# Optimization experiments

Hardware: AMD Instinct MI355X
Metric: run time of the kernel (lower is better)

The kernel has to match this reference:

```python
import jax, jax.numpy as jnp
import numpy as np

N = 50000
E = 800000
IN_C, HID, OUT_C = 128, 64, 64
L = 8
ALPHA, THETA = 0.1, 0.5


def setup_inputs() -> dict:
    key = jax.random.key(0)
    ks = jax.random.split(key, 7)
    x = jax.random.normal(ks[0], (N, IN_C), dtype=jnp.float32)
    edge_index = jax.random.randint(ks[1], (2, E), 0, N, dtype=jnp.int64)
    # parameters (Linear weights stored [out, in] like torch)
    w_in = jax.random.normal(ks[2], (HID, IN_C), dtype=jnp.float32) / np.sqrt(IN_C)
    b_in = jnp.zeros((HID,), dtype=jnp.float32)
    conv_w = jax.random.normal(ks[3], (L, HID, HID), dtype=jnp.float32) / np.sqrt(HID)
    w_out = jax.random.normal(ks[4], (OUT_C, HID), dtype=jnp.float32) / np.sqrt(HID)
    b_out = jnp.zeros((OUT_C,), dtype=jnp.float32)
    return {"x": x, "edge_index": edge_index, "w_in": w_in, "b_in": b_in,
            "conv_w": conv_w, "w_out": w_out, "b_out": b_out}


def reference(x, edge_index, w_in, b_in, conv_w, w_out, b_out):
    # add self loops
    loops = jnp.arange(N, dtype=edge_index.dtype)
    row = jnp.concatenate([edge_index[0], loops])
    col = jnp.concatenate([edge_index[1], loops])
    # symmetric GCN normalization from in-degree of col
    deg = jax.ops.segment_sum(jnp.ones_like(col, dtype=x.dtype), col, num_segments=N)
    dinv = jnp.where(deg > 0, jax.lax.rsqrt(deg), 0.0)
    norm = (dinv[row] * dinv[col])[:, None]  # [E+N, 1]

    # eval mode: dropout is identity
    h = jax.nn.relu(x @ w_in.T + b_in)
    x0 = h
    betas = jnp.log(THETA / jnp.arange(1, L + 1, dtype=jnp.float32) + 1.0)

    def layer(h, wb):
        W, beta = wb
        agg = jax.ops.segment_sum(h[row] * norm, col, num_segments=N)  # gather-scale-scatter
        agg = (1.0 - ALPHA) * agg + ALPHA * x0                         # initial residual
        out = (1.0 - beta) * agg + beta * (agg @ W.T)                  # identity mapping
        return jax.nn.relu(out), None

    h, _ = jax.lax.scan(layer, h, (conv_w, betas))
    return h @ w_out.T + b_out
```

## Files before the change

kernel.cpp:

```cpp
#include <hip/hip_runtime.h>
#include <math.h>

#define NN 50000
#define EE 800000
#define INC 128
#define HIDC 64
#define OUTC 64
#define LLAYERS 8
#define TOT (EE + NN)
#define NB 196
#define ABLK 256
#define CHUNKA ((TOT + ABLK - 1) / ABLK)

#define WAVE_LDS_FENCE() asm volatile("s_waitcnt lgkmcnt(0)" ::: "memory")

typedef __attribute__((ext_vector_type(8))) short bf16x8;
typedef __attribute__((ext_vector_type(4))) float f32x4;

__device__ __forceinline__ float bf2f(unsigned short u) {
    return __uint_as_float(((unsigned int)u) << 16);
}
__device__ __forceinline__ unsigned short f2bf(float f) {
    unsigned int u = __float_as_uint(f);
    u += 0x7FFFu + ((u >> 16) & 1u);
    return (unsigned short)(u >> 16);
}

__global__ void detect_kernel(const long long* __restrict__ p, int* __restrict__ flag) {
    long long v = p[threadIdx.x];
    if (v < 0 || v >= NN) atomicOr(flag, 1);
}

__device__ __forceinline__ int load_row(const void* ei, int is64, int e) {
    return is64 ? (int)((const long long*)ei)[e] : ((const int*)ei)[e];
}
__device__ __forceinline__ int load_col(const void* ei, int is64, int e) {
    return is64 ? (int)((const long long*)ei)[EE + e] : ((const int*)ei)[EE + e];
}

__global__ __launch_bounds__(256) void histA(const void* __restrict__ ei,
                                             const int* __restrict__ flag,
                                             int* __restrict__ bcnt) {
    __shared__ int h[NB];
    int tid = threadIdx.x;
    for (int i = tid; i < NB; i += 256) h[i] = 0;
    __syncthreads();
    int is64 = (*flag == 0);
    int lo = blockIdx.x * CHUNKA, hi = lo + CHUNKA; if (hi > TOT) hi = TOT;
    for (int e = lo + tid; e < hi; e += 256) {
        int c = (e < EE) ? load_col(ei, is64, e) : (e - EE);
        atomicAdd(&h[c >> 8], 1);
    }
    __syncthreads();
    for (int i = tid; i < NB; i += 256) if (h[i]) atomicAdd(&bcnt[i], h[i]);
}

__global__ __launch_bounds__(256) void scan_buckets(const int* __restrict__ bcnt,
                                                    int* __restrict__ bstart,
                                                    int* __restrict__ bcur) {
    __shared__ int s[256];
    int t = threadIdx.x;
    int v = (t < NB) ? bcnt[t] : 0;
    s[t] = v;
    __syncthreads();
    for (int off = 1; off < 256; off <<= 1) {
        int a = (t >= off) ? s[t - off] : 0;
        __syncthreads();
        s[t] += a;
        __syncthreads();
    }
    if (t < NB) { int st = s[t] - v; bstart[t] = st; bcur[t] = st; }
    if (t == NB - 1) bstart[NB] = s[t];
}

__global__ __launch_bounds__(256) void bucket_scatter(const void* __restrict__ ei,
                                                      const int* __restrict__ flag,
                                                      int* __restrict__ bcur,
                                                      unsigned int* __restrict__ barr) {
    __shared__ int h[NB];
    __shared__ int base[NB];
    int tid = threadIdx.x;
    for (int i = tid; i < NB; i += 256) h[i] = 0;
    __syncthreads();
    int is64 = (*flag == 0);
    int lo = blockIdx.x * CHUNKA, hi = lo + CHUNKA; if (hi > TOT) hi = TOT;
    for (int e = lo + tid; e < hi; e += 256) {
        int c = (e < EE) ? load_col(ei, is64, e) : (e - EE);
        atomicAdd(&h[c >> 8], 1);
    }
    __syncthreads();
    for (int i = tid; i < NB; i += 256) {
        int cnt = h[i];
        base[i] = cnt ? atomicAdd(&bcur[i], cnt) : 0;
        h[i] = 0;
    }
    __syncthreads();
    for (int e = lo + tid; e < hi; e += 256) {
        int r, c;
        if (e < EE) { r = load_row(ei, is64, e); c = load_col(ei, is64, e); }
        else        { r = e - EE; c = r; }
        int b = c >> 8;
        int p = base[b] + atomicAdd(&h[b], 1);
        barr[p] = ((unsigned int)r << 8) | (unsigned int)(c & 255);
    }
}

__global__ __launch_bounds__(256) void bucket_offsets(const unsigned int* __restrict__ barr,
                                                      const int* __restrict__ bstart,
                                                      int* __restrict__ offsets,
                                                      float* __restrict__ dinv) {
    __shared__ int cnt[256];
    __shared__ int pre[256];
    int b = blockIdx.x, t = threadIdx.x;
    cnt[t] = 0;
    __syncthreads();
    int lo = bstart[b], hi = bstart[b + 1];
    for (int i = lo + t; i < hi; i += 256) atomicAdd(&cnt[barr[i] & 255u], 1);
    __syncthreads();
    int v = cnt[t];
    pre[t] = v;
    __syncthreads();
    for (int off = 1; off < 256; off <<= 1) {
        int a = (t >= off) ? pre[t - off] : 0;
        __syncthreads();
        pre[t] += a;
        __syncthreads();
    }
    int c = (b << 8) + t;
    if (c <= NN) offsets[c] = bstart[b] + pre[t] - v;
    if (c < NN)  dinv[c] = 1.0f / sqrtf((float)v);
}

__global__ __launch_bounds__(256) void bucket_place(const unsigned int* __restrict__ barr,
                                                    const int* __restrict__ bstart,
                                                    const int* __restrict__ offsets,
                                                    const float* __restrict__ dinv,
                                                    int2* __restrict__ adj) {
    __shared__ int cur[256];
    int b = blockIdx.x, t = threadIdx.x;
    int c0 = b << 8;
    int c = c0 + t;
    cur[t] = (c < NN) ? offsets[c] : 0;
    __syncthreads();
    int lo = bstart[b], hi = bstart[b + 1];
    for (int i = lo + t; i < hi; i += 256) {
        unsigned int v = barr[i];
        int r = (int)(v >> 8);
        int ci = (int)(v & 255u);
        int pos = atomicAdd(&cur[ci], 1);
        adj[pos] = make_int2(r, __float_as_int(dinv[r] * dinv[c0 + ci]));
    }
}

__global__ __launch_bounds__(256) void in_gemm(const float* __restrict__ x,
                                               const float* __restrict__ w_in,
                                               const float* __restrict__ b_in,
                                               unsigned short* __restrict__ h,
                                               float* __restrict__ x0) {
    __shared__ unsigned short xT[16 * 136];
    int tid = threadIdx.x, w = tid >> 6, lane = tid & 63;
    int g = lane >> 4, c = lane & 15;
    int base = blockIdx.x << 4;

    bf16x8 bfrag[4];
    {
        const float* Wrow = w_in + (size_t)((w << 4) + c) * INC;
        #pragma unroll
        for (int kt = 0; kt < 4; ++kt) {
            int k0 = kt * 32 + (g << 3);
            float4 va = *reinterpret_cast<const float4*>(Wrow + k0);
            float4 vb = *reinterpret_cast<const float4*>(Wrow + k0 + 4);
            bf16x8 r;
            r[0] = (short)f2bf(va.x); r[1] = (short)f2bf(va.y);
            r[2] = (short)f2bf(va.z); r[3] = (short)f2bf(va.w);
            r[4] = (short)f2bf(vb.x); r[5] = (short)f2bf(vb.y);
            r[6] = (short)f2bf(vb.z); r[7] = (short)f2bf(vb.w);
            bfrag[kt] = r;
        }
    }

    #pragma unroll
    for (int m = 0; m < 2; ++m) {
        int idx = tid * 2 + m;
        int row = idx >> 5, col4 = idx & 31;
        float4 v = *reinterpret_cast<const float4*>(
            x + (((size_t)(base + row)) << 7) + (col4 << 2));
        ushort4 pk;
        pk.x = f2bf(v.x); pk.y = f2bf(v.y); pk.z = f2bf(v.z); pk.w = f2bf(v.w);
        *reinterpret_cast<ushort4*>(&xT[row * 136 + (col4 << 2)]) = pk;
    }
    __syncthreads();

    f32x4 d = {0.f, 0.f, 0.f, 0.f};
    #pragma unroll
    for (int kt = 0; kt < 4; ++kt) {
        bf16x8 a = *reinterpret_cast<const bf16x8*>(&xT[c * 136 + kt * 32 + (g << 3)]);
        d = __builtin_amdgcn_mfma_f32_16x16x32_bf16(a, bfrag[kt], d, 0, 0, 0);
    }
    float bj = b_in[(w << 4) + c];
    #pragma unroll
    for (int r = 0; r < 4; ++r) {
        int node = base + (g << 2) + r;
        int ch = (w << 4) + c;
        float v = fmaxf(d[r] + bj, 0.0f);
        h[((size_t)node << 6) + ch]  = f2bf(v);
        x0[((size_t)node << 6) + ch] = v;
    }
}

__global__ __launch_bounds__(256) void layer_mfma(
        const unsigned short* __restrict__ h_in, unsigned short* __restrict__ h_out,
        const float* __restrict__ x0,
        const int* __restrict__ offsets, const int2* __restrict__ adj,
        const float* __restrict__ W, float beta) {
    __shared__ unsigned short WtL[64 * 72];
    __shared__ unsigned short aggT[4][16 * 72];
    int tid = threadIdx.x, w = tid >> 6, lane = tid & 63;
    int g = lane >> 4, c = lane & 15;
    float omb = 1.0f - beta;

    for (int i = tid; i < HIDC * HIDC; i += 256) {
        int n = i >> 6, k = i & 63;
        float t = beta * W[i] + ((k == n) ? omb : 0.0f);
        WtL[n * 72 + k] = f2bf(t);
    }
    __syncthreads();

    int base = blockIdx.x << 4;
    int n = base + (w << 2) + g;
    int e0 = offsets[n], e1 = offsets[n + 1];
    float4 acc = make_float4(0.f, 0.f, 0.f, 0.f);
    int e = e0;
    for (; e + 4 <= e1; e += 4) {
        int2 a0 = adj[e], a1 = adj[e + 1], a2 = adj[e + 2], a3 = adj[e + 3];
        ushort4 h0 = *reinterpret_cast<const ushort4*>(h_in + ((a0.x << 6) + (c << 2)));
        ushort4 h1 = *reinterpret_cast<const ushort4*>(h_in + ((a1.x << 6) + (c << 2)));
        ushort4 h2 = *reinterpret_cast<const ushort4*>(h_in + ((a2.x << 6) + (c << 2)));
        ushort4 h3 = *reinterpret_cast<const ushort4*>(h_in + ((a3.x << 6) + (c << 2)));
        float n0 = __int_as_float(a0.y), n1 = __int_as_float(a1.y);
        float n2 = __int_as_float(a2.y), n3 = __int_as_float(a3.y);
        acc.x = fmaf(n0, bf2f(h0.x), acc.x); acc.y = fmaf(n0, bf2f(h0.y), acc.y);
        acc.z = fmaf(n0, bf2f(h0.z), acc.z); acc.w = fmaf(n0, bf2f(h0.w), acc.w);
        acc.x = fmaf(n1, bf2f(h1.x), acc.x); acc.y = fmaf(n1, bf2f(h1.y), acc.y);
        acc.z = fmaf(n1, bf2f(h1.z), acc.z); acc.w = fmaf(n1, bf2f(h1.w), acc.w);
        acc.x = fmaf(n2, bf2f(h2.x), acc.x); acc.y = fmaf(n2, bf2f(h2.y), acc.y);
        acc.z = fmaf(n2, bf2f(h2.z), acc.z); acc.w = fmaf(n2, bf2f(h2.w), acc.w);
        acc.x = fmaf(n3, bf2f(h3.x), acc.x); acc.y = fmaf(n3, bf2f(h3.y), acc.y);
        acc.z = fmaf(n3, bf2f(h3.z), acc.z); acc.w = fmaf(n3, bf2f(h3.w), acc.w);
    }
    for (; e < e1; ++e) {
        int2 a = adj[e];
        ushort4 hv = *reinterpret_cast<const ushort4*>(h_in + ((a.x << 6) + (c << 2)));
        float nrm = __int_as_float(a.y);
        acc.x = fmaf(nrm, bf2f(hv.x), acc.x);
        acc.y = fmaf(nrm, bf2f(hv.y), acc.y);
        acc.z = fmaf(nrm, bf2f(hv.z), acc.z);
        acc.w = fmaf(nrm, bf2f(hv.w), acc.w);
    }
    {
        const float4 x0v = *reinterpret_cast<const float4*>(x0 + ((n << 6) + (c << 2)));
        ushort4 pk;
        pk.x = f2bf(fmaf(0.9f, acc.x, 0.1f * x0v.x));
        pk.y = f2bf(fmaf(0.9f, acc.y, 0.1f * x0v.y));
        pk.z = f2bf(fmaf(0.9f, acc.z, 0.1f * x0v.z));
        pk.w = f2bf(fmaf(0.9f, acc.w, 0.1f * x0v.w));
        *reinterpret_cast<ushort4*>(&aggT[w][g * 72 + (c << 2)]) = pk;
    }
    WAVE_LDS_FENCE();

    bf16x8 afrag0 = *reinterpret_cast<const bf16x8*>(&aggT[w][c * 72 + (g << 3)]);
    bf16x8 afrag1 = *reinterpret_cast<const bf16x8*>(&aggT[w][c * 72 + 32 + (g << 3)]);

    #pragma unroll
    for (int t = 0; t < 4; ++t) {
        bf16x8 b0 = *reinterpret_cast<const bf16x8*>(
            &WtL[((t << 4) + c) * 72 + (g << 3)]);
        bf16x8 b1 = *reinterpret_cast<const bf16x8*>(
            &WtL[((t << 4) + c) * 72 + 32 + (g << 3)]);
        f32x4 d = {0.f, 0.f, 0.f, 0.f};
        d = __builtin_amdgcn_mfma_f32_16x16x32_bf16(afrag0, b0, d, 0, 0, 0);
        d = __builtin_amdgcn_mfma_f32_16x16x32_bf16(afrag1, b1, d, 0, 0, 0);
        if (g == 0) {
            #pragma unroll
            for (int r = 0; r < 4; ++r) {
                int node = base + (w << 2) + r;
                int ch = (t << 4) + c;
                h_out[(node << 6) + ch] = f2bf(fmaxf(d[r], 0.0f));
            }
        }
    }
}

__global__ __launch_bounds__(256, 8) void out_gemm(const unsigned short* __restrict__ h,
                                                   const float* __restrict__ w_out,
                                                   const float* __restrict__ b_out,
                                                   float* __restrict__ out) {
    __shared__ float4 WI4[16 * HIDC];
    __shared__ float  vecs[4][HIDC];
    int tid = threadIdx.x;
    const float4* W4 = reinterpret_cast<const float4*>(w_out);
    for (int m = 0; m < 4; ++m) {
        int idx = tid + m * 256;
        int s = idx >> 6, j = idx & 63;
        WI4[idx] = W4[j * 16 + s];
    }
    __syncthreads();
    int w = tid >> 6, lane = tid & 63;
    float bj = b_out[lane];
    for (int n0 = blockIdx.x * 4; n0 < NN; n0 += gridDim.x * 4) {
        int n = n0 + w;
        if (n < NN) {
            vecs[w][lane] = bf2f(h[(n << 6) + lane]);
            WAVE_LDS_FENCE();
            float acc = bj;
            #pragma unroll
            for (int s = 0; s < 16; ++s) {
                float4 wv = WI4[(s << 6) + lane];
                float4 vv = *reinterpret_cast<const float4*>(&vecs[w][s << 2]);
                acc = fmaf(wv.x, vv.x, acc);
                acc = fmaf(wv.y, vv.y, acc);
                acc = fmaf(wv.z, vv.z, acc);
                acc = fmaf(wv.w, vv.w, acc);
            }
            out[(n << 6) + lane] = acc;
        }
    }
}

extern "C" void kernel_launch(void* const* d_in, const int* in_sizes, int n_in,
                              void* d_out, int out_size, void* d_ws, size_t ws_size,
                              hipStream_t stream) {
    const float* x      = (const float*)d_in[0];
    const void*  ei     = d_in[1];
    const float* w_in   = (const float*)d_in[2];
    const float* b_in   = (const float*)d_in[3];
    const float* conv_w = (const float*)d_in[4];
    const float* w_out  = (const float*)d_in[5];
    const float* b_out  = (const float*)d_in[6];
    float* out = (float*)d_out;

    char* ws = (char*)d_ws;
    size_t off = 0;
    auto alloc = [&](size_t bytes) -> void* {
        void* p = ws + off;
        off += (bytes + 255) & ~(size_t)255;
        return p;
    };
    int*   flag    = (int*)alloc(4);
    float* dinv    = (float*)alloc((size_t)NN * 4);
    int*   offsets = (int*)alloc((size_t)(NN + 1) * 4);
    int*   bcnt    = (int*)alloc((size_t)NB * 4);
    int*   bstart  = (int*)alloc((size_t)(NB + 1) * 4);
    int*   bcur    = (int*)alloc((size_t)NB * 4);
    int2*  adj     = (int2*)alloc((size_t)TOT * 8);
    unsigned short* hA = (unsigned short*)alloc((size_t)NN * HIDC * 2);
    unsigned short* hB = (unsigned short*)alloc((size_t)NN * HIDC * 2);
    float* x0      = (float*)alloc((size_t)NN * HIDC * 4);
    unsigned int* barr = (unsigned int*)hA;

    hipMemsetAsync(flag, 0, 4, stream);
    hipMemsetAsync(bcnt, 0, (size_t)NB * 4, stream);
    detect_kernel<<<1, 256, 0, stream>>>((const long long*)ei, flag);
    histA<<<ABLK, 256, 0, stream>>>(ei, flag, bcnt);
    scan_buckets<<<1, 256, 0, stream>>>(bcnt, bstart, bcur);
    bucket_scatter<<<ABLK, 256, 0, stream>>>(ei, flag, bcur, barr);
    bucket_offsets<<<NB, 256, 0, stream>>>(barr, bstart, offsets, dinv);
    bucket_place<<<NB, 256, 0, stream>>>(barr, bstart, offsets, dinv, adj);
    in_gemm<<<NN / 16, 256, 0, stream>>>(x, w_in, b_in, hA, x0);

    unsigned short* cur = hA;
    unsigned short* nxt = hB;
    for (int l = 0; l < LLAYERS; ++l) {
        float beta = logf(0.5f / (float)(l + 1) + 1.0f);
        const float* Wl = conv_w + (size_t)l * HIDC * HIDC;
        layer_mfma<<<NN / 16, 256, 0, stream>>>(cur, nxt, x0, offsets, adj, Wl, beta);
        unsigned short* t = cur; cur = nxt; nxt = t;
    }
    out_gemm<<<1024, 256, 0, stream>>>(cur, w_out, b_out, out);
}
```

Before: 286.0 us.

## Precompute bf16 layer weights once and load MFMA B fragments from global

Adds a one-time kernel that folds beta and the identity term into bf16 weights for all layers. Each layer block then loads its B fragments straight into registers from global memory instead of rebuilding a 64x64 LDS tile with a block barrier in every one of its 3125 blocks. The layer kernel's occupancy hint is raised to 8, and the output projection is rewritten to use MFMA over 16-node tiles instead of scalar FMA dot products. The cost is one extra launch and more registers per thread held for the weight fragments.

```diff
diff --git a/kernel.cpp b/kernel.cpp
--- a/kernel.cpp
+++ b/kernel.cpp
@@ -150,6 +150,17 @@
         int pos = atomicAdd(&cur[ci], 1);
         adj[pos] = make_int2(r, __float_as_int(dinv[r] * dinv[c0 + ci]));
     }
+}
+
+__global__ __launch_bounds__(256) void wt_prep(const float* __restrict__ conv_w,
+                                               unsigned short* __restrict__ wtg) {
+    int idx = blockIdx.x * 256 + threadIdx.x;
+    if (idx >= LLAYERS * HIDC * HIDC) return;
+    int l = idx >> 12, i = idx & 4095;
+    int n = i >> 6, k = i & 63;
+    float beta = logf(0.5f / (float)(l + 1) + 1.0f);
+    float t = beta * conv_w[idx] + ((k == n) ? (1.0f - beta) : 0.0f);
+    wtg[idx] = f2bf(t);
 }
 
 __global__ __launch_bounds__(256) void in_gemm(const float* __restrict__ x,
@@ -208,23 +219,22 @@
     }
 }
 
-__global__ __launch_bounds__(256) void layer_mfma(
+__global__ __launch_bounds__(256, 8) void layer_mfma(
         const unsigned short* __restrict__ h_in, unsigned short* __restrict__ h_out,
         const float* __restrict__ x0,
         const int* __restrict__ offsets, const int2* __restrict__ adj,
-        const float* __restrict__ W, float beta) {
-    __shared__ unsigned short WtL[64 * 72];
+        const unsigned short* __restrict__ wt) {
     __shared__ unsigned short aggT[4][16 * 72];
     int tid = threadIdx.x, w = tid >> 6, lane = tid & 63;
     int g = lane >> 4, c = lane & 15;
-    float omb = 1.0f - beta;
-
-    for (int i = tid; i < HIDC * HIDC; i += 256) {
-        int n = i >> 6, k = i & 63;
-        float t = beta * W[i] + ((k == n) ? omb : 0.0f);
-        WtL[n * 72 + k] = f2bf(t);
-    }
-    __syncthreads();
+
+    bf16x8 bfrag[4][2];
+    #pragma unroll
+    for (int t = 0; t < 4; ++t) {
+        const unsigned short* row = wt + (((t << 4) + c) << 6) + (g << 3);
+        bfrag[t][0] = *reinterpret_cast<const bf16x8*>(row);
+        bfrag[t][1] = *reinterpret_cast<const bf16x8*>(row + 32);
+    }
 
     int base = blockIdx.x << 4;
     int n = base + (w << 2) + g;
@@ -273,13 +283,9 @@
 
     #pragma unroll
     for (int t = 0; t < 4; ++t) {
-        bf16x8 b0 = *reinterpret_cast<const bf16x8*>(
-            &WtL[((t << 4) + c) * 72 + (g << 3)]);
-        bf16x8 b1 = *reinterpret_cast<const bf16x8*>(
-            &WtL[((t << 4) + c) * 72 + 32 + (g << 3)]);
         f32x4 d = {0.f, 0.f, 0.f, 0.f};
-        d = __builtin_amdgcn_mfma_f32_16x16x32_bf16(afrag0, b0, d, 0, 0, 0);
-        d = __builtin_amdgcn_mfma_f32_16x16x32_bf16(afrag1, b1, d, 0, 0, 0);
+        d = __builtin_amdgcn_mfma_f32_16x16x32_bf16(afrag0, bfrag[t][0], d, 0, 0, 0);
+        d = __builtin_amdgcn_mfma_f32_16x16x32_bf16(afrag1, bfrag[t][1], d, 0, 0, 0);
         if (g == 0) {
             #pragma unroll
             for (int r = 0; r < 4; ++r) {
@@ -291,39 +297,52 @@
     }
 }
 
-__global__ __launch_bounds__(256, 8) void out_gemm(const unsigned short* __restrict__ h,
-                                                   const float* __restrict__ w_out,
-                                                   const float* __restrict__ b_out,
-                                                   float* __restrict__ out) {
-    __shared__ float4 WI4[16 * HIDC];
-    __shared__ float  vecs[4][HIDC];
-    int tid = threadIdx.x;
-    const float4* W4 = reinterpret_cast<const float4*>(w_out);
-    for (int m = 0; m < 4; ++m) {
-        int idx = tid + m * 256;
-        int s = idx >> 6, j = idx & 63;
-        WI4[idx] = W4[j * 16 + s];
-    }
-    __syncthreads();
-    int w = tid >> 6, lane = tid & 63;
-    float bj = b_out[lane];
-    for (int n0 = blockIdx.x * 4; n0 < NN; n0 += gridDim.x * 4) {
-        int n = n0 + w;
-        if (n < NN) {
-            vecs[w][lane] = bf2f(h[(n << 6) + lane]);
-            WAVE_LDS_FENCE();
-            float acc = bj;
-            #pragma unroll
-            for (int s = 0; s < 16; ++s) {
-                float4 wv = WI4[(s << 6) + lane];
-                float4 vv = *reinterpret_cast<const float4*>(&vecs[w][s << 2]);
-                acc = fmaf(wv.x, vv.x, acc);
-                acc = fmaf(wv.y, vv.y, acc);
-                acc = fmaf(wv.z, vv.z, acc);
-                acc = fmaf(wv.w, vv.w, acc);
-            }
-            out[(n << 6) + lane] = acc;
+__global__ __launch_bounds__(256) void out_gemm(const unsigned short* __restrict__ h,
+                                                const float* __restrict__ w_out,
+                                                const float* __restrict__ b_out,
+                                                float* __restrict__ out) {
+    __shared__ unsigned short hT[16 * 72];
+    int tid = threadIdx.x, w = tid >> 6, lane = tid & 63;
+    int g = lane >> 4, c = lane & 15;
+    int base = blockIdx.x << 4;
+
+    bf16x8 bfrag[2];
+    {
+        const float* Wrow = w_out + (size_t)((w << 4) + c) * HIDC;
+        #pragma unroll
+        for (int kt = 0; kt < 2; ++kt) {
+            int k0 = kt * 32 + (g << 3);
+            float4 va = *reinterpret_cast<const float4*>(Wrow + k0);
+            float4 vb = *reinterpret_cast<const float4*>(Wrow + k0 + 4);
+            bf16x8 r;
+            r[0] = (short)f2bf(va.x); r[1] = (short)f2bf(va.y);
+            r[2] = (short)f2bf(va.z); r[3] = (short)f2bf(va.w);
+            r[4] = (short)f2bf(vb.x); r[5] = (short)f2bf(vb.y);
+            r[6] = (short)f2bf(vb.z); r[7] = (short)f2bf(vb.w);
+            bfrag[kt] = r;
         }
+    }
+
+    {
+        int row = tid >> 4, col4 = tid & 15;
+        ushort4 v = *reinterpret_cast<const ushort4*>(
+            h + ((size_t)(base + row) << 6) + (col4 << 2));
+        *reinterpret_cast<ushort4*>(&hT[row * 72 + (col4 << 2)]) = v;
+    }
+    __syncthreads();
+
+    bf16x8 a0 = *reinterpret_cast<const bf16x8*>(&hT[c * 72 + (g << 3)]);
+    bf16x8 a1 = *reinterpret_cast<const bf16x8*>(&hT[c * 72 + 32 + (g << 3)]);
+    f32x4 d = {0.f, 0.f, 0.f, 0.f};
+    d = __builtin_amdgcn_mfma_f32_16x16x32_bf16(a0, bfrag[0], d, 0, 0, 0);
+    d = __builtin_amdgcn_mfma_f32_16x16x32_bf16(a1, bfrag[1], d, 0, 0, 0);
+
+    float bj = b_out[(w << 4) + c];
+    #pragma unroll
+    for (int r = 0; r < 4; ++r) {
+        int node = base + (g << 2) + r;
+        int ch = (w << 4) + c;
+        out[((size_t)node << 6) + ch] = d[r] + bj;
     }
 }
 
@@ -352,6 +371,7 @@
     int*   bcnt    = (int*)alloc((size_t)NB * 4);
     int*   bstart  = (int*)alloc((size_t)(NB + 1) * 4);
     int*   bcur    = (int*)alloc((size_t)NB * 4);
+    unsigned short* wtg = (unsigned short*)alloc((size_t)LLAYERS * HIDC * HIDC * 2);
     int2*  adj     = (int2*)alloc((size_t)TOT * 8);
     unsigned short* hA = (unsigned short*)alloc((size_t)NN * HIDC * 2);
     unsigned short* hB = (unsigned short*)alloc((size_t)NN * HIDC * 2);
@@ -366,15 +386,15 @@
     bucket_scatter<<<ABLK, 256, 0, stream>>>(ei, flag, bcur, barr);
     bucket_offsets<<<NB, 256, 0, stream>>>(barr, bstart, offsets, dinv);
     bucket_place<<<NB, 256, 0, stream>>>(barr, bstart, offsets, dinv, adj);
+    wt_prep<<<(LLAYERS * HIDC * HIDC + 255) / 256, 256, 0, stream>>>(conv_w, wtg);
     in_gemm<<<NN / 16, 256, 0, stream>>>(x, w_in, b_in, hA, x0);
 
     unsigned short* cur = hA;
     unsigned short* nxt = hB;
     for (int l = 0; l < LLAYERS; ++l) {
-        float beta = logf(0.5f / (float)(l + 1) + 1.0f);
-        const float* Wl = conv_w + (size_t)l * HIDC * HIDC;
-        layer_mfma<<<NN / 16, 256, 0, stream>>>(cur, nxt, x0, offsets, adj, Wl, beta);
+        const unsigned short* wtl = wtg + (size_t)l * HIDC * HIDC;
+        layer_mfma<<<NN / 16, 256, 0, stream>>>(cur, nxt, x0, offsets, adj, wtl);
         unsigned short* t = cur; cur = nxt; nxt = t;
     }
-    out_gemm<<<1024, 256, 0, stream>>>(cur, w_out, b_out, out);
-}
+    out_gemm<<<NN / 16, 256, 0, stream>>>(cur, w_out, b_out, out);
+}
```

After: 390.7 us. 36.6% more time.
